# Kernel tuning notes

Hardware: AMD Instinct MI355X
Metric: run time of the kernel (lower is better)

Reference implementation:

```python
import jax, jax.numpy as jnp
import numpy as np

N_NODES = 50000
N_EDGES = 800000
IN_CH = 128
OUT_CH = 64
SELF_LOOP_W = 2.0  # improved=True in GCNConv


def setup_inputs() -> dict:
    key = jax.random.key(0)
    k1, k2, k3, k4 = jax.random.split(key, 4)
    x = jax.random.normal(k1, (N_NODES, IN_CH), dtype=jnp.float32)
    edge_index = jax.random.randint(k2, (2, N_EDGES), 0, N_NODES, dtype=jnp.int64)
    edge_weight = jax.random.uniform(k3, (N_EDGES,), dtype=jnp.float32)
    W = jax.random.normal(k4, (IN_CH, OUT_CH), dtype=jnp.float32) / np.sqrt(IN_CH)
    b = jnp.zeros((OUT_CH,), dtype=jnp.float32)
    return {"x": x, "edge_index": edge_index, "edge_weight": edge_weight, "W": W, "b": b}


def reference(x, edge_index, edge_weight, W, b):
    # Only the first GCNConv layer runs (the torch loop returns after k=0).
    N = x.shape[0]
    row, col = edge_index[0], edge_index[1]  # source, target

    # gcn_norm with add_self_loops=True, improved=True (fill value 2.0)
    loop_idx = jnp.arange(N, dtype=edge_index.dtype)
    row_f = jnp.concatenate([row, loop_idx])
    col_f = jnp.concatenate([col, loop_idx])
    ew_f = jnp.concatenate([edge_weight, jnp.full((N,), SELF_LOOP_W, dtype=edge_weight.dtype)])

    deg = jax.ops.segment_sum(ew_f, col_f, num_segments=N)          # [N]
    dinv = jnp.where(deg > 0, jax.lax.rsqrt(deg), 0.0)
    norm = dinv[row_f] * ew_f * dinv[col_f]                          # [E+N]

    # linear transform then normalized sparse aggregation
    xw = x @ W                                                       # [N, out]
    msg = norm[:, None] * xw[row_f]                                  # [E+N, out] gather
    out = jax.ops.segment_sum(msg, col_f, num_segments=N)           # [N, out] scatter-add
    return out + b
```

## Files before the change

kernel.cpp:

```cpp
#include <hip/hip_runtime.h>

constexpr int N    = 50000;
constexpr int E    = 800000;
constexpr int CIN  = 128;
constexpr int COUT = 64;
constexpr float SELF_LOOP_W = 2.0f;

constexpr int NB   = (N + 63) / 64;
constexpr int CAP  = 1536;
constexpr int EPB  = 4096;
constexpr int PBLK = (E + EPB - 1) / EPB;

typedef float          vfloat4  __attribute__((ext_vector_type(4)));
typedef float          vfloat2  __attribute__((ext_vector_type(2)));
typedef int            vint2    __attribute__((ext_vector_type(2)));
typedef unsigned short vushort4 __attribute__((ext_vector_type(4)));

__device__ __forceinline__ unsigned short f2bf(float f) {
    unsigned int u = __float_as_uint(f);
    u += 0x7FFFu + ((u >> 16) & 1u);
    return (unsigned short)(u >> 16);
}
__device__ __forceinline__ float bf2f(unsigned short h) {
    return __uint_as_float(((unsigned int)h) << 16);
}
__device__ __forceinline__ vfloat2 bf2x(unsigned int u) {
    vfloat2 f;
    f.x = __uint_as_float(u << 16);
    f.y = __uint_as_float(u & 0xFFFF0000u);
    return f;
}

__global__ void init_kernel(int* __restrict__ bcur) {
    int i = blockIdx.x * blockDim.x + threadIdx.x;
    if (i < NB) bcur[i] = i * CAP;
}

__global__ __launch_bounds__(512) void partition_kernel(const int* __restrict__ row,
                                                        const int* __restrict__ col,
                                                        const float* __restrict__ ew,
                                                        int* __restrict__ bcur,
                                                        vint2* __restrict__ pk) {
    __shared__ int lhist[NB];
    __shared__ int lbase[NB];
    const int t  = threadIdx.x;
    const int e0 = blockIdx.x * EPB;

    for (int i = t; i < NB; i += 512) lhist[i] = 0;
    __syncthreads();

    #pragma unroll
    for (int k = 0; k < EPB / 512; ++k) {
        int e = e0 + k * 512 + t;
        if (e < E) atomicAdd(&lhist[col[e] >> 6], 1);
    }
    __syncthreads();

    for (int i = t; i < NB; i += 512) {
        int h = lhist[i];
        lbase[i] = (h > 0) ? atomicAdd(&bcur[i], h) : 0;
    }
    __syncthreads();
    for (int i = t; i < NB; i += 512) lhist[i] = 0;
    __syncthreads();

    #pragma unroll
    for (int k = 0; k < EPB / 512; ++k) {
        int e = e0 + k * 512 + t;
        if (e < E) {
            int c   = col[e];
            int bkt = c >> 6;
            int p = lbase[bkt] + atomicAdd(&lhist[bkt], 1);
            if (p < (bkt + 1) * CAP) {
                vint2 v;
                v.x = row[e] | ((c & 63) << 20);
                v.y = __float_as_int(ew[e]);
                pk[p] = v;
            }
        }
    }
}

__global__ __launch_bounds__(256) void deg_kernel(const int* __restrict__ bcur,
                                                  const vint2* __restrict__ pk,
                                                  float* __restrict__ dinv) {
    __shared__ float ldeg[64];
    const int t    = threadIdx.x;
    const int b    = blockIdx.x;
    const int base = b * CAP;
    const int cnt  = min(bcur[b] - base, CAP);

    if (t < 64) ldeg[t] = 0.f;
    __syncthreads();
    for (int j = t; j < cnt; j += 256) {
        vint2 v = pk[base + j];
        atomicAdd(&ldeg[(v.x >> 20) & 63], __int_as_float(v.y));
    }
    __syncthreads();
    int node = b * 64 + t;
    if (t < 64 && node < N) dinv[node] = rsqrtf(SELF_LOOP_W + ldeg[t]);
}

__global__ __launch_bounds__(256) void xw_kernel(const float* __restrict__ x,
                                                 const float* __restrict__ W,
                                                 unsigned short* __restrict__ xwh) {
    __shared__ __align__(16) float xs[64][132];

    const int t    = threadIdx.x;
    const int base = blockIdx.x * 64;

    #pragma unroll
    for (int i = 0; i < 8; ++i) {
        int f4  = i * 256 + t;
        int r   = f4 >> 5;
        int c4  = f4 & 31;
        int node = base + r;
        if (node >= N) node = N - 1;
        vfloat4 v = *(const vfloat4*)(x + (size_t)node * CIN + c4 * 4);
        *(vfloat4*)&xs[r][c4 * 4] = v;
    }
    __syncthreads();

    const int tc = t & 15;
    const int tn = t >> 4;

    float acc[4][4];
    #pragma unroll
    for (int i = 0; i < 4; ++i)
        #pragma unroll
        for (int j = 0; j < 4; ++j) acc[i][j] = 0.f;

    const float* Wp = W + tc * 4;
    #pragma unroll 8
    for (int k = 0; k < CIN; ++k) {
        vfloat4 bv = *(const vfloat4*)(Wp + (size_t)k * COUT);
        float a0 = xs[tn * 4 + 0][k];
        float a1 = xs[tn * 4 + 1][k];
        float a2 = xs[tn * 4 + 2][k];
        float a3 = xs[tn * 4 + 3][k];
        #pragma unroll
        for (int j = 0; j < 4; ++j) {
            acc[0][j] += a0 * bv[j];
            acc[1][j] += a1 * bv[j];
            acc[2][j] += a2 * bv[j];
            acc[3][j] += a3 * bv[j];
        }
    }

    #pragma unroll
    for (int i = 0; i < 4; ++i) {
        int node = base + tn * 4 + i;
        if (node >= N) continue;
        vushort4 hv;
        #pragma unroll
        for (int j = 0; j < 4; ++j) hv[j] = f2bf(acc[i][j]);
        *(vushort4*)(xwh + (size_t)node * COUT + tc * 4) = hv;
    }
}

__global__ __launch_bounds__(512) void aggregate_kernel(const int* __restrict__ bcur,
                                                        const vint2* __restrict__ pk,
                                                        const float* __restrict__ dinv,
                                                        const unsigned short* __restrict__ xwh,
                                                        const float* __restrict__ bias,
                                                        float* __restrict__ out) {
    __shared__ int   rawx[CAP];
    __shared__ float rawn[CAP];
    __shared__ int   s_r[CAP];
    __shared__ float s_n[CAP];
    __shared__ int   lhist[64], lofs[64], lcur[64];

    const int t    = threadIdx.x;
    const int lane = t & 63;
    const int wv   = t >> 6;
    const int b    = blockIdx.x;
    const int base = b * CAP;
    const int cnt  = min(bcur[b] - base, CAP);

    if (t < 64) lhist[t] = 0;
    __syncthreads();

    for (int j = t; j < cnt; j += 512) {
        vint2 v = pk[base + j];
        rawx[j] = v.x;
        rawn[j] = __int_as_float(v.y) * dinv[v.x & 0xFFFFF];
        atomicAdd(&lhist[(v.x >> 20) & 63], 1);
    }
    __syncthreads();

    if (t < 64) {
        int v = lhist[t];
        int s = v;
        #pragma unroll
        for (int d = 1; d < 64; d <<= 1) {
            int u = __shfl_up(s, d);
            if (lane >= d) s += u;
        }
        lofs[t] = s - v;
        lcur[t] = s - v;
    }
    __syncthreads();

    for (int j = t; j < cnt; j += 512) {
        int xv = rawx[j];
        int p  = atomicAdd(&lcur[(xv >> 20) & 63], 1);
        s_r[p] = xv & 0xFFFFF;
        s_n[p] = rawn[j];
    }
    __syncthreads();

    const int half = lane >> 5;
    const int c2   = lane & 31;

    for (int nd = wv; nd < 64; nd += 8) {
        int node = b * 64 + nd;
        if (node >= N) continue;
        int s0 = lofs[nd];
        int e0 = s0 + lhist[nd];
        float ax = 0.f, ay = 0.f;

        for (int i = s0; i < e0; i += 16) {
            int rr[8]; float nn[8]; unsigned int vv[8];
            #pragma unroll
            for (int u = 0; u < 8; ++u) {
                int j = i + 2 * u + half;
                bool ok = (j < e0);
                rr[u] = ok ? s_r[j] : s_r[s0];
                nn[u] = ok ? s_n[j] : 0.f;
            }
            #pragma unroll
            for (int u = 0; u < 8; ++u)
                vv[u] = *(const unsigned int*)(xwh + (size_t)rr[u] * COUT + c2 * 2);
            #pragma unroll
            for (int u = 0; u < 8; ++u) {
                vfloat2 f = bf2x(vv[u]);
                ax += nn[u] * f.x;
                ay += nn[u] * f.y;
            }
        }
        ax += __shfl_xor(ax, 32);
        ay += __shfl_xor(ay, 32);

        if (half == 0) {
            float dc = dinv[node];
            unsigned int su = *(const unsigned int*)(xwh + (size_t)node * COUT + c2 * 2);
            vfloat2 sf = bf2x(su);
            vfloat2 o;
            o.x = dc * ax + SELF_LOOP_W * dc * dc * sf.x + bias[c2 * 2];
            o.y = dc * ay + SELF_LOOP_W * dc * dc * sf.y + bias[c2 * 2 + 1];
            *(vfloat2*)(out + (size_t)node * COUT + c2 * 2) = o;
        }
    }
}

extern "C" void kernel_launch(void* const* d_in, const int* in_sizes, int n_in,
                              void* d_out, int out_size, void* d_ws, size_t ws_size,
                              hipStream_t stream) {
    const float* x  = (const float*)d_in[0];
    const int*   ei = (const int*)d_in[1];
    const float* ew = (const float*)d_in[2];
    const float* W  = (const float*)d_in[3];
    const float* b  = (const float*)d_in[4];
    float* out = (float*)d_out;

    unsigned short* xwh  = (unsigned short*)d_ws;
    float*          dinv = (float*)(xwh + (size_t)N * COUT);
    int*            bcur = (int*)(dinv + N);
    vint2*          pk   = (vint2*)(bcur + NB + 2);

    const int* rowp = ei;
    const int* colp = ei + E;

    init_kernel     <<<(NB + 255) / 256, 256, 0, stream>>>(bcur);
    partition_kernel<<<PBLK, 512, 0, stream>>>(rowp, colp, ew, bcur, pk);
    xw_kernel       <<<NB, 256, 0, stream>>>(x, W, xwh);
    deg_kernel      <<<NB, 256, 0, stream>>>(bcur, pk, dinv);
    aggregate_kernel<<<NB, 512, 0, stream>>>(bcur, pk, dinv, xwh, b, out);
}
```

Before: 147.9 us.

## Fuse degree into xw kernel, memset bucket counters, widen aggregate gathers to 8 bytes

Merges the degree/rsqrt computation into the x@W kernel, so there is one launch fewer and the packed-edge read overlaps GEMM work. The init kernel is replaced by hipMemsetAsync, with bucket counters now holding relative offsets instead of absolute positions. The aggregation loop switches from 4-byte to 8-byte bf16 gathers per lane (16 lanes per row, 4 edges per iteration), with a two-step shuffle reduction and a vectorized output store. The wider gathers should cut memory instructions, at the cost of fewer edges in flight per lane and an extra shuffle stage.

```diff
diff --git a/kernel.cpp b/kernel.cpp
--- a/kernel.cpp
+++ b/kernel.cpp
@@ -12,7 +12,6 @@
 constexpr int PBLK = (E + EPB - 1) / EPB;
 
 typedef float          vfloat4  __attribute__((ext_vector_type(4)));
-typedef float          vfloat2  __attribute__((ext_vector_type(2)));
 typedef int            vint2    __attribute__((ext_vector_type(2)));
 typedef unsigned short vushort4 __attribute__((ext_vector_type(4)));
 
@@ -23,17 +22,6 @@
 }
 __device__ __forceinline__ float bf2f(unsigned short h) {
     return __uint_as_float(((unsigned int)h) << 16);
-}
-__device__ __forceinline__ vfloat2 bf2x(unsigned int u) {
-    vfloat2 f;
-    f.x = __uint_as_float(u << 16);
-    f.y = __uint_as_float(u & 0xFFFF0000u);
-    return f;
-}
-
-__global__ void init_kernel(int* __restrict__ bcur) {
-    int i = blockIdx.x * blockDim.x + threadIdx.x;
-    if (i < NB) bcur[i] = i * CAP;
 }
 
 __global__ __launch_bounds__(512) void partition_kernel(const int* __restrict__ row,
@@ -58,7 +46,7 @@
 
     for (int i = t; i < NB; i += 512) {
         int h = lhist[i];
-        lbase[i] = (h > 0) ? atomicAdd(&bcur[i], h) : 0;
+        if (h > 0) lbase[i] = i * CAP + atomicAdd(&bcur[i], h);
     }
     __syncthreads();
     for (int i = t; i < NB; i += 512) lhist[i] = 0;
@@ -81,33 +69,18 @@
     }
 }
 
-__global__ __launch_bounds__(256) void deg_kernel(const int* __restrict__ bcur,
-                                                  const vint2* __restrict__ pk,
-                                                  float* __restrict__ dinv) {
+__global__ __launch_bounds__(256) void xw_deg_kernel(const float* __restrict__ x,
+                                                     const float* __restrict__ W,
+                                                     const int* __restrict__ bcur,
+                                                     const vint2* __restrict__ pk,
+                                                     unsigned short* __restrict__ xwh,
+                                                     float* __restrict__ dinv) {
+    __shared__ __align__(16) float xs[64][132];
     __shared__ float ldeg[64];
+
     const int t    = threadIdx.x;
     const int b    = blockIdx.x;
-    const int base = b * CAP;
-    const int cnt  = min(bcur[b] - base, CAP);
-
-    if (t < 64) ldeg[t] = 0.f;
-    __syncthreads();
-    for (int j = t; j < cnt; j += 256) {
-        vint2 v = pk[base + j];
-        atomicAdd(&ldeg[(v.x >> 20) & 63], __int_as_float(v.y));
-    }
-    __syncthreads();
-    int node = b * 64 + t;
-    if (t < 64 && node < N) dinv[node] = rsqrtf(SELF_LOOP_W + ldeg[t]);
-}
-
-__global__ __launch_bounds__(256) void xw_kernel(const float* __restrict__ x,
-                                                 const float* __restrict__ W,
-                                                 unsigned short* __restrict__ xwh) {
-    __shared__ __align__(16) float xs[64][132];
-
-    const int t    = threadIdx.x;
-    const int base = blockIdx.x * 64;
+    const int base = b * 64;
 
     #pragma unroll
     for (int i = 0; i < 8; ++i) {
@@ -119,6 +92,7 @@
         vfloat4 v = *(const vfloat4*)(x + (size_t)node * CIN + c4 * 4);
         *(vfloat4*)&xs[r][c4 * 4] = v;
     }
+    if (t < 64) ldeg[t] = 0.f;
     __syncthreads();
 
     const int tc = t & 15;
@@ -156,6 +130,16 @@
         for (int j = 0; j < 4; ++j) hv[j] = f2bf(acc[i][j]);
         *(vushort4*)(xwh + (size_t)node * COUT + tc * 4) = hv;
     }
+
+    const int pbase = b * CAP;
+    const int cnt   = min(bcur[b], CAP);
+    for (int j = t; j < cnt; j += 256) {
+        vint2 v = pk[pbase + j];
+        atomicAdd(&ldeg[(v.x >> 20) & 63], __int_as_float(v.y));
+    }
+    __syncthreads();
+    int node = base + t;
+    if (t < 64 && node < N) dinv[node] = rsqrtf(SELF_LOOP_W + ldeg[t]);
 }
 
 __global__ __launch_bounds__(512) void aggregate_kernel(const int* __restrict__ bcur,
@@ -175,7 +159,7 @@
     const int wv   = t >> 6;
     const int b    = blockIdx.x;
     const int base = b * CAP;
-    const int cnt  = min(bcur[b] - base, CAP);
+    const int cnt  = min(bcur[b], CAP);
 
     if (t < 64) lhist[t] = 0;
     __syncthreads();
@@ -209,46 +193,52 @@
     }
     __syncthreads();
 
-    const int half = lane >> 5;
-    const int c2   = lane & 31;
+    const int q  = lane >> 4;
+    const int c4 = lane & 15;
 
     for (int nd = wv; nd < 64; nd += 8) {
         int node = b * 64 + nd;
         if (node >= N) continue;
         int s0 = lofs[nd];
         int e0 = s0 + lhist[nd];
-        float ax = 0.f, ay = 0.f;
-
+
+        float a0 = 0.f, a1 = 0.f, a2 = 0.f, a3 = 0.f;
         for (int i = s0; i < e0; i += 16) {
-            int rr[8]; float nn[8]; unsigned int vv[8];
+            int rr[4]; float nn[4]; vushort4 vv[4];
             #pragma unroll
-            for (int u = 0; u < 8; ++u) {
-                int j = i + 2 * u + half;
+            for (int u = 0; u < 4; ++u) {
+                int j = i + 4 * u + q;
                 bool ok = (j < e0);
                 rr[u] = ok ? s_r[j] : s_r[s0];
                 nn[u] = ok ? s_n[j] : 0.f;
             }
             #pragma unroll
-            for (int u = 0; u < 8; ++u)
-                vv[u] = *(const unsigned int*)(xwh + (size_t)rr[u] * COUT + c2 * 2);
+            for (int u = 0; u < 4; ++u)
+                vv[u] = *(const vushort4*)(xwh + (size_t)rr[u] * COUT + c4 * 4);
             #pragma unroll
-            for (int u = 0; u < 8; ++u) {
-                vfloat2 f = bf2x(vv[u]);
-                ax += nn[u] * f.x;
-                ay += nn[u] * f.y;
+            for (int u = 0; u < 4; ++u) {
+                a0 += nn[u] * bf2f(vv[u][0]);
+                a1 += nn[u] * bf2f(vv[u][1]);
+                a2 += nn[u] * bf2f(vv[u][2]);
+                a3 += nn[u] * bf2f(vv[u][3]);
             }
         }
-        ax += __shfl_xor(ax, 32);
-        ay += __shfl_xor(ay, 32);
-
-        if (half == 0) {
+        a0 += __shfl_xor(a0, 16); a0 += __shfl_xor(a0, 32);
+        a1 += __shfl_xor(a1, 16); a1 += __shfl_xor(a1, 32);
+        a2 += __shfl_xor(a2, 16); a2 += __shfl_xor(a2, 32);
+        a3 += __shfl_xor(a3, 16); a3 += __shfl_xor(a3, 32);
+
+        if (q == 0) {
             float dc = dinv[node];
-            unsigned int su = *(const unsigned int*)(xwh + (size_t)node * COUT + c2 * 2);
-            vfloat2 sf = bf2x(su);
-            vfloat2 o;
-            o.x = dc * ax + SELF_LOOP_W * dc * dc * sf.x + bias[c2 * 2];
-            o.y = dc * ay + SELF_LOOP_W * dc * dc * sf.y + bias[c2 * 2 + 1];
-            *(vfloat2*)(out + (size_t)node * COUT + c2 * 2) = o;
+            float s2 = SELF_LOOP_W * dc * dc;
+            vushort4 sh = *(const vushort4*)(xwh + (size_t)node * COUT + c4 * 4);
+            vfloat4  bv = *(const vfloat4*)(bias + c4 * 4);
+            vfloat4  o;
+            o[0] = dc * a0 + s2 * bf2f(sh[0]) + bv[0];
+            o[1] = dc * a1 + s2 * bf2f(sh[1]) + bv[1];
+            o[2] = dc * a2 + s2 * bf2f(sh[2]) + bv[2];
+            o[3] = dc * a3 + s2 * bf2f(sh[3]) + bv[3];
+            *(vfloat4*)(out + (size_t)node * COUT + c4 * 4) = o;
         }
     }
 }
@@ -271,9 +261,8 @@
     const int* rowp = ei;
     const int* colp = ei + E;
 
-    init_kernel     <<<(NB + 255) / 256, 256, 0, stream>>>(bcur);
+    hipMemsetAsync(bcur, 0, NB * sizeof(int), stream);
     partition_kernel<<<PBLK, 512, 0, stream>>>(rowp, colp, ew, bcur, pk);
-    xw_kernel       <<<NB, 256, 0, stream>>>(x, W, xwh);
-    deg_kernel      <<<NB, 256, 0, stream>>>(bcur, pk, dinv);
+    xw_deg_kernel   <<<NB, 256, 0, stream>>>(x, W, bcur, pk, xwh, dinv);
     aggregate_kernel<<<NB, 512, 0, stream>>>(bcur, pk, dinv, xwh, b, out);
 }
```

Result: no change. 146.6 us (-0.9%).
